# Kernel optimization log

Hardware: AMD Instinct MI355X
Metric: run time of the kernel (lower is better)

The kernel has to match this reference:

```python
import jax, jax.numpy as jnp
import numpy as np
from jax import lax

EPS = 1e-5  # BatchNorm1d default eps

def setup_inputs() -> dict:
    key = jax.random.key(0)
    ks = jax.random.split(key, 8)
    B, IN, H, T = 1024, 128, 256, 256
    return {
        "inputs": jax.random.normal(ks[0], (B, IN), jnp.float32),
        "hidden": jnp.zeros((B, H), jnp.float32),
        "W_ih": jax.random.normal(ks[1], (3 * H, IN), jnp.float32) * 0.05,
        "b_ih": jax.random.normal(ks[2], (3 * H,), jnp.float32) * 0.05,
        "W_hh": jax.random.normal(ks[3], (3 * H, H), jnp.float32) * 0.05,
        "b_hh": jax.random.normal(ks[4], (3 * H,), jnp.float32) * 0.05,
        "W_lin": jax.random.normal(ks[5], (IN, H), jnp.float32) * 0.05,
        "b_lin": jax.random.normal(ks[6], (IN,), jnp.float32) * 0.05,
        "n_frames": 256,
    }

def reference(inputs, hidden, W_ih, b_ih, W_hh, b_hh, W_lin, b_lin, n_frames):
    def step(carry, _):
        x, h = carry
        gi = x @ W_ih.T + b_ih          # [B, 3H]
        gh = h @ W_hh.T + b_hh          # [B, 3H]
        i_r, i_z, i_n = jnp.split(gi, 3, axis=-1)
        h_r, h_z, h_n = jnp.split(gh, 3, axis=-1)
        r = jax.nn.sigmoid(i_r + h_r)
        z = jax.nn.sigmoid(i_z + h_z)
        n = jnp.tanh(i_n + r * h_n)
        h_new = (1.0 - z) * n + z * h   # GRUCell update
        y = h_new @ W_lin.T + b_lin     # fed back as next input
        return (y, h_new), y

    _, ys = lax.scan(step, (inputs, hidden), None, length=n_frames)  # [T, B, out]
    # BatchNorm1d(affine=False), training mode: biased batch stats per timestep
    mean = jnp.mean(ys, axis=1, keepdims=True)
    var = jnp.var(ys, axis=1, keepdims=True)
    return (ys - mean) / jnp.sqrt(var + EPS)
```

## Files before the change

kernel.cpp:

```cpp
#include <hip/hip_runtime.h>


typedef _Float16 half8 __attribute__((ext_vector_type(8)));
typedef float floatx4 __attribute__((ext_vector_type(4)));
typedef unsigned uintx4 __attribute__((ext_vector_type(4)));

#define EPS_BN 1e-5f

#define WS_WC 0
#define WS_W0 524288
#define WS_WL 1114112
#define WS_B0 1179648
#define WS_BC 1183744
#define WS_ST 1187840

static __device__ __forceinline__ unsigned short f2h(float f) {
    union { _Float16 h; unsigned short u; } v;
    v.h = (_Float16)f;
    return v.u;
}
static __device__ __forceinline__ half8 as_h8(uint4 v) {
    union { uint4 u; half8 h; } x; x.u = v; return x.h;
}
static __device__ __forceinline__ half8 ld_agpr(const uint4* p) {
    uintx4 v = *(const uintx4*)p;
    asm volatile("; wpin" : "+a"(v));
    union { uintx4 u; half8 h; } x; x.u = v; return x.h;
}
static __device__ __forceinline__ float sigm(float x) {
    return 1.0f / (1.0f + __expf(-x));
}
static __device__ __forceinline__ float tanh_fast(float x) {
    return 1.0f - 2.0f / (__expf(2.0f * x) + 1.0f);
}
#define MFMA16(A, B, C) __builtin_amdgcn_mfma_f32_16x16x32_f16((A), (B), (C), 0, 0, 0)

__global__ void pack_w0_kernel(const float* __restrict__ W_ih, const float* __restrict__ W_hh,
                               const float* __restrict__ W_lin, const float* __restrict__ b_ih,
                               const float* __restrict__ b_hh,
                               uint4* __restrict__ w0, uint4* __restrict__ wl,
                               float4* __restrict__ bias0)
{
    int i = blockIdx.x * 256 + threadIdx.x;
    if (i < 36864) {
        int lane = i & 63, tile = i >> 6;
        int w = tile / 36, rem = tile - w * 36;
        int g = rem / 12, kt = rem - g * 12;
        int n = g * 256 + (w << 4) + (lane & 15);
        int k0 = (kt << 5) + ((lane >> 4) << 3);
        const float* p = (k0 < 128) ? (W_ih + n * 128 + k0)
                                    : (W_hh + n * 256 + (k0 - 128));
        unsigned short h[8];
        #pragma unroll
        for (int j = 0; j < 8; ++j) h[j] = f2h(p[j]);
        uint4 v;
        v.x = (unsigned)h[0] | ((unsigned)h[1] << 16);
        v.y = (unsigned)h[2] | ((unsigned)h[3] << 16);
        v.z = (unsigned)h[4] | ((unsigned)h[5] << 16);
        v.w = (unsigned)h[6] | ((unsigned)h[7] << 16);
        w0[i] = v;
    } else if (i < 40960) {
        int i2 = i - 36864;
        int lane = i2 & 63, tile = i2 >> 6;
        int n = (tile >> 3) * 16 + (lane & 15);
        int k0 = ((tile & 7) << 5) + ((lane >> 4) << 3);
        const float* p = W_lin + n * 256 + k0;
        unsigned short h[8];
        #pragma unroll
        for (int j = 0; j < 8; ++j) h[j] = f2h(p[j]);
        uint4 v;
        v.x = (unsigned)h[0] | ((unsigned)h[1] << 16);
        v.y = (unsigned)h[2] | ((unsigned)h[3] << 16);
        v.z = (unsigned)h[4] | ((unsigned)h[5] << 16);
        v.w = (unsigned)h[6] | ((unsigned)h[7] << 16);
        wl[i2] = v;
    } else if (i < 41216) {
        int cb = i - 40960;
        bias0[cb] = make_float4(b_ih[cb] + b_hh[cb],
                                b_ih[256 + cb] + b_hh[256 + cb],
                                b_ih[512 + cb], b_hh[512 + cb]);
    }
}

__global__ void pack_wc_kernel(const float* __restrict__ W_ih, const float* __restrict__ W_hh,
                               const float* __restrict__ W_lin, const float* __restrict__ b_ih,
                               const float* __restrict__ b_hh, const float* __restrict__ b_lin,
                               uint4* __restrict__ wc, float4* __restrict__ bc)
{
    int i = blockIdx.x * 256 + threadIdx.x;
    if (i < 32768) {
        int lane = i & 63, tile = i >> 6;
        int w = tile >> 5, r = tile & 31;
        int g = r >> 3, kt = r & 7;
        int c = (w << 4) + (lane & 15);
        int k0 = (kt << 5) + ((lane >> 4) << 3);
        float s[8];
        if (g == 3) {
            #pragma unroll
            for (int j = 0; j < 8; ++j) s[j] = W_hh[(512 + c) * 256 + k0 + j];
        } else {
            int row = g * 256 + c;
            const float* wi = W_ih + row * 128;
            #pragma unroll
            for (int j = 0; j < 8; ++j) s[j] = 0.0f;
            for (int ii = 0; ii < 128; ++ii) {
                float wv = wi[ii];
                const float* wrow = W_lin + ii * 256 + k0;
                #pragma unroll
                for (int j = 0; j < 8; ++j) s[j] += wv * wrow[j];
            }
            if (g < 2) {
                #pragma unroll
                for (int j = 0; j < 8; ++j) s[j] += W_hh[row * 256 + k0 + j];
            }
        }
        unsigned short h[8];
        #pragma unroll
        for (int j = 0; j < 8; ++j) h[j] = f2h(s[j]);
        uint4 v;
        v.x = (unsigned)h[0] | ((unsigned)h[1] << 16);
        v.y = (unsigned)h[2] | ((unsigned)h[3] << 16);
        v.z = (unsigned)h[4] | ((unsigned)h[5] << 16);
        v.w = (unsigned)h[6] | ((unsigned)h[7] << 16);
        wc[i] = v;
    } else if (i < 33024) {
        int c = i - 32768;
        float d0 = 0.f, d1 = 0.f, d2 = 0.f;
        for (int ii = 0; ii < 128; ++ii) {
            float bl = b_lin[ii];
            d0 += bl * W_ih[c * 128 + ii];
            d1 += bl * W_ih[(256 + c) * 128 + ii];
            d2 += bl * W_ih[(512 + c) * 128 + ii];
        }
        bc[c] = make_float4(b_ih[c] + b_hh[c] + d0,
                            b_ih[256 + c] + b_hh[256 + c] + d1,
                            b_ih[512 + c] + d2,
                            b_hh[512 + c]);
    }
}

__global__ __launch_bounds__(512, 2) void gru_kernel(
    const float* __restrict__ inputs,
    const float* __restrict__ hidden,
    const uint4* __restrict__ wc,
    const uint4* __restrict__ w0,
    const float4* __restrict__ bias0,
    const float4* __restrict__ bcp,
    float* __restrict__ out)
{
    __shared__ uint4 lds[9472];

    const int tid  = threadIdx.x;
    const int lane = tid & 63;
    const int w    = tid >> 6;
    const int quad = lane >> 4;
    const int nc   = lane & 15;
    const int r0   = blockIdx.x << 4;
    const int c0   = (w << 4) + nc;
    const int c1   = 128 + c0;
    const float4 bc0 = bcp[c0];
    const float4 bc1 = bcp[c1];
    const uint4* wcw0 = wc + (size_t)w * 2048;
    const uint4* wcw1 = wc + (size_t)(w + 8) * 2048;

    half8 wr0[8], wz0[8], wr1[8], wz1[8];
    #pragma unroll
    for (int kt = 0; kt < 8; ++kt) {
        wr0[kt] = ld_agpr(&wcw0[kt * 64 + lane]);
        wz0[kt] = ld_agpr(&wcw0[(8 + kt) * 64 + lane]);
        wr1[kt] = ld_agpr(&wcw1[kt * 64 + lane]);
        wz1[kt] = ld_agpr(&wcw1[(8 + kt) * 64 + lane]);
    }

    const int wbase = 1280 + (w << 10);
    #pragma unroll
    for (int i = 0; i < 8; ++i) {
        lds[wbase + (i << 6) + lane]       = wcw0[(18 + i) * 64 + lane];
        lds[wbase + 512 + (i << 6) + lane] = wcw1[(18 + i) * 64 + lane];
    }

    float hreg[8];
    #pragma unroll
    for (int d = 0; d < 4; ++d) {
        hreg[d]     = hidden[(r0 + (quad << 2) + d) * 256 + c0];
        hreg[4 + d] = hidden[(r0 + (quad << 2) + d) * 256 + c1];
    }

    unsigned short* lds_u16 = (unsigned short*)lds;
    const int kp  = ((w & 1) << 4) + nc;
    const int lf  = ((kp >> 3) << 4) + (quad << 2);
    const int hfb0 = (((w >> 1) * 64 + lf) << 3) + (kp & 7);
    const int hfb1 = (((4 + (w >> 1)) * 64 + lf) << 3) + (kp & 7);

    for (int idx = tid; idx < 2048; idx += 512) {
        int ktl = idx >> 8;
        int rem = idx & 255;
        int lfr = rem >> 2, jg = rem & 3;
        int m = lfr & 15;
        int hc = ktl * 32 + (lfr >> 4) * 8 + jg * 2;
        const float* p = hidden + (r0 + m) * 256 + hc;
        unsigned pk = (unsigned)f2h(p[0]) | ((unsigned)f2h(p[1]) << 16);
        ((unsigned*)lds)[(ktl * 64 + lfr) * 4 + jg] = pk;
    }
    for (int idx = tid; idx < 1024; idx += 512) {
        int kt = idx >> 8, lfr = (idx >> 2) & 63, jg = idx & 3;
        int m = lfr & 15;
        int k0 = (kt << 5) + ((lfr >> 4) << 3) + (jg << 1);
        const float* p = inputs + (r0 + m) * 128 + k0;
        unsigned pk = (unsigned)f2h(p[0]) | ((unsigned)f2h(p[1]) << 16);
        ((unsigned*)lds)[(1024 + (kt << 6) + lfr) * 4 + jg] = pk;
    }
    __syncthreads();

    unsigned short* Hout = (unsigned short*)out;

    {
        #pragma unroll
        for (int g2 = 0; g2 < 2; ++g2) {
            const uint4* ww = w0 + (size_t)(g2 ? (w + 8) : w) * 2304;
            floatx4 ar = {0.f,0.f,0.f,0.f}, az = {0.f,0.f,0.f,0.f};
            floatx4 ain = {0.f,0.f,0.f,0.f}, ahn = {0.f,0.f,0.f,0.f};
            #pragma unroll
            for (int kt = 0; kt < 12; ++kt) {
                half8 A = as_h8(kt < 4 ? lds[1024 + (kt << 6) + lane]
                                       : lds[((kt - 4) << 6) + lane]);
                ar = MFMA16(A, as_h8(ww[kt * 64 + lane]), ar);
                az = MFMA16(A, as_h8(ww[(12 + kt) * 64 + lane]), az);
                if (kt < 4)
                    ain = MFMA16(A, as_h8(ww[(24 + kt) * 64 + lane]), ain);
                else
                    ahn = MFMA16(A, as_h8(ww[(24 + kt) * 64 + lane]), ahn);
            }
            const int cc = g2 ? c1 : c0;
            const int hfb = g2 ? hfb1 : hfb0;
            float4 b0 = bias0[cc];
            #pragma unroll
            for (int d = 0; d < 4; ++d) {
                float rr = sigm(ar[d] + b0.x);
                float zz = sigm(az[d] + b0.y);
                float nn = tanh_fast(ain[d] + b0.z + rr * (ahn[d] + b0.w));
                float hnew = (1.0f - zz) * nn + zz * hreg[(g2 << 2) + d];
                hreg[(g2 << 2) + d] = hnew;
                unsigned short hu = f2h(hnew);
                lds_u16[4096 + hfb + (d << 3)] = hu;
                Hout[((size_t)(r0 + (quad << 2) + d) << 8) + cc] = hu;
            }
        }
        __syncthreads();
    }

    for (int t = 1; t < 256; ++t) {
        const int rb   = (t & 1) << 9;
        const int wb16 = (((t + 1) & 1) << 9) << 3;

        const uint4* s0p = wcw0 + lane;
        const uint4* s1p = wcw1 + lane;
        asm("" : "+v"(s0p), "+v"(s1p));

        uint4 a_i0 = s0p[16 * 64], a_i1 = s0p[17 * 64];
        uint4 a_h2 = s0p[26 * 64], a_h3 = s0p[27 * 64];
        uint4 b_i0 = s1p[16 * 64], b_i1 = s1p[17 * 64];
        uint4 b_h2 = s1p[26 * 64], b_h3 = s1p[27 * 64];

        floatx4 ar0 = {0.f,0.f,0.f,0.f}, az0 = {0.f,0.f,0.f,0.f};
        floatx4 ai0 = {0.f,0.f,0.f,0.f}, ah0 = {0.f,0.f,0.f,0.f};
        floatx4 ar1 = {0.f,0.f,0.f,0.f}, az1 = {0.f,0.f,0.f,0.f};
        floatx4 ai1 = {0.f,0.f,0.f,0.f}, ah1 = {0.f,0.f,0.f,0.f};

        uint4 a_h4, a_h5, a_h6, a_h7, b_h4, b_h5, b_h6, b_h7;

        #pragma unroll
        for (int kt = 0; kt < 8; ++kt) {
            half8 A = as_h8(lds[rb + (kt << 6) + lane]);
            if (kt == 1) {
                a_h4 = s0p[28 * 64]; b_h4 = s1p[28 * 64];
                a_h5 = s0p[29 * 64]; b_h5 = s1p[29 * 64];
            }
            if (kt == 3) {
                a_h6 = s0p[30 * 64]; b_h6 = s1p[30 * 64];
                a_h7 = s0p[31 * 64]; b_h7 = s1p[31 * 64];
            }
            ar0 = MFMA16(A, wr0[kt], ar0);
            ar1 = MFMA16(A, wr1[kt], ar1);
            az0 = MFMA16(A, wz0[kt], az0);
            az1 = MFMA16(A, wz1[kt], az1);
            half8 Bi0 = (kt == 0) ? as_h8(a_i0) : (kt == 1) ? as_h8(a_i1)
                       : as_h8(lds[wbase + ((kt - 2) << 6) + lane]);
            half8 Bi1 = (kt == 0) ? as_h8(b_i0) : (kt == 1) ? as_h8(b_i1)
                       : as_h8(lds[wbase + 512 + ((kt - 2) << 6) + lane]);
            ai0 = MFMA16(A, Bi0, ai0);
            ai1 = MFMA16(A, Bi1, ai1);
            half8 Bh0 = (kt < 2)  ? as_h8(lds[wbase + ((6 + kt) << 6) + lane])
                       : (kt == 2) ? as_h8(a_h2) : (kt == 3) ? as_h8(a_h3)
                       : (kt == 4) ? as_h8(a_h4) : (kt == 5) ? as_h8(a_h5)
                       : (kt == 6) ? as_h8(a_h6) : as_h8(a_h7);
            half8 Bh1 = (kt < 2)  ? as_h8(lds[wbase + 512 + ((6 + kt) << 6) + lane])
                       : (kt == 2) ? as_h8(b_h2) : (kt == 3) ? as_h8(b_h3)
                       : (kt == 4) ? as_h8(b_h4) : (kt == 5) ? as_h8(b_h5)
                       : (kt == 6) ? as_h8(b_h6) : as_h8(b_h7);
            ah0 = MFMA16(A, Bh0, ah0);
            ah1 = MFMA16(A, Bh1, ah1);
        }

        const size_t obase = (size_t)t * 1024 + r0 + (quad << 2);
        #pragma unroll
        for (int d = 0; d < 4; ++d) {
            float rr = sigm(ar0[d] + bc0.x);
            float zz = sigm(az0[d] + bc0.y);
            float nn = tanh_fast(ai0[d] + bc0.z + rr * (ah0[d] + bc0.w));
            float hnew = (1.0f - zz) * nn + zz * hreg[d];
            hreg[d] = hnew;
            unsigned short hu = f2h(hnew);
            lds_u16[wb16 + hfb0 + (d << 3)] = hu;
            Hout[((obase + d) << 8) + c0] = hu;
        }
        #pragma unroll
        for (int d = 0; d < 4; ++d) {
            float rr = sigm(ar1[d] + bc1.x);
            float zz = sigm(az1[d] + bc1.y);
            float nn = tanh_fast(ai1[d] + bc1.z + rr * (ah1[d] + bc1.w));
            float hnew = (1.0f - zz) * nn + zz * hreg[4 + d];
            hreg[4 + d] = hnew;
            unsigned short hu = f2h(hnew);
            lds_u16[wb16 + hfb1 + (d << 3)] = hu;
            Hout[((obase + d) << 8) + c1] = hu;
        }
        __syncthreads();
    }
}

__global__ __launch_bounds__(256) void ygemm_kernel(
    const uint4* __restrict__ wl, const float* __restrict__ b_lin,
    float* __restrict__ out, float* __restrict__ stats)
{
    __shared__ unsigned short sh[16 * 264];
    const int tid = threadIdx.x;
    const int t = blockIdx.x >> 6;
    const int r0 = (blockIdx.x & 63) << 4;

    {
        int row = tid >> 4, seg = tid & 15;
        const uint4* src = (const uint4*)((const unsigned short*)out
                         + (((size_t)t << 10) + r0 + row) * 256) + (seg << 1);
        uint4 a = src[0], b = src[1];
        uint4* dst = (uint4*)(sh + row * 264 + (seg << 4));
        dst[0] = a; dst[1] = b;
    }
    __syncthreads();

    const int lane = tid & 63, w = tid >> 6;
    const int quad = lane >> 4, nc = lane & 15;
    const int m = lane & 15, khi = lane >> 4;

    half8 B0[8], B1[8];
    #pragma unroll
    for (int kt = 0; kt < 8; ++kt) {
        B0[kt] = as_h8(wl[(((w << 1) + 0) * 8 + kt) * 64 + lane]);
        B1[kt] = as_h8(wl[(((w << 1) + 1) * 8 + kt) * 64 + lane]);
    }
    floatx4 a0 = {0.f,0.f,0.f,0.f}, a1 = {0.f,0.f,0.f,0.f};
    #pragma unroll
    for (int kt = 0; kt < 8; ++kt) {
        half8 A = *(const half8*)(sh + m * 264 + (kt << 5) + (khi << 3));
        a0 = MFMA16(A, B0[kt], a0);
        a1 = MFMA16(A, B1[kt], a1);
    }
    #pragma unroll
    for (int g = 0; g < 2; ++g) {
        floatx4 acc = g ? a1 : a0;
        int i = (((w << 1) + g) << 4) + nc;
        float bl = b_lin[i];
        float s1 = 0.f, s2 = 0.f;
        float* orow = out + (((size_t)t << 10) + r0 + (quad << 2)) * 128 + i;
        #pragma unroll
        for (int d = 0; d < 4; ++d) {
            float y = acc[d] + bl;
            orow[(size_t)d << 7] = y;
            s1 += y; s2 += y * y;
        }
        s1 += __shfl_xor(s1, 16); s1 += __shfl_xor(s1, 32);
        s2 += __shfl_xor(s2, 16); s2 += __shfl_xor(s2, 32);
        if (lane < 16) {
            int si = ((t << 7) + (((w << 1) + g) << 4) + lane) << 1;
            atomicAdd(&stats[si], s1);
            atomicAdd(&stats[si + 1], s2);
        }
    }
}

__global__ void norm_kernel(float* __restrict__ out, const float* __restrict__ stats)
{
    __shared__ float smean[128], sscale[128];
    int t = blockIdx.x >> 2, q = blockIdx.x & 3;
    int tid = threadIdx.x;
    if (tid < 128) {
        int si = ((t << 7) + tid) << 1;
        float mean = stats[si] * (1.0f / 1024.0f);
        float var = stats[si + 1] * (1.0f / 1024.0f) - mean * mean;
        smean[tid] = mean;
        sscale[tid] = rsqrtf(var + EPS_BN);
    }
    __syncthreads();
    float4* p = (float4*)(out + ((size_t)t << 17) + ((size_t)q << 15));
    for (int i = tid; i < 8192; i += 256) {
        int cc = (i & 31) << 2;
        float4 v = p[i];
        v.x = (v.x - smean[cc])     * sscale[cc];
        v.y = (v.y - smean[cc + 1]) * sscale[cc + 1];
        v.z = (v.z - smean[cc + 2]) * sscale[cc + 2];
        v.w = (v.w - smean[cc + 3]) * sscale[cc + 3];
        p[i] = v;
    }
}

extern "C" void kernel_launch(void* const* d_in, const int* in_sizes, int n_in,
                              void* d_out, int out_size, void* d_ws, size_t ws_size,
                              hipStream_t stream) {
    (void)in_sizes; (void)n_in; (void)out_size; (void)ws_size;
    const float* inputs = (const float*)d_in[0];
    const float* hidden = (const float*)d_in[1];
    const float* W_ih   = (const float*)d_in[2];
    const float* b_ih   = (const float*)d_in[3];
    const float* W_hh   = (const float*)d_in[4];
    const float* b_hh   = (const float*)d_in[5];
    const float* W_lin  = (const float*)d_in[6];
    const float* b_lin  = (const float*)d_in[7];

    char* ws = (char*)d_ws;
    uint4*  wcp   = (uint4*)(ws + WS_WC);
    uint4*  w0p   = (uint4*)(ws + WS_W0);
    uint4*  wlp   = (uint4*)(ws + WS_WL);
    float4* bias0 = (float4*)(ws + WS_B0);
    float4* bcp   = (float4*)(ws + WS_BC);
    float*  stats = (float*)(ws + WS_ST);

    hipMemsetAsync(stats, 0, 262144, stream);
    pack_w0_kernel<<<161, 256, 0, stream>>>(W_ih, W_hh, W_lin, b_ih, b_hh, w0p, wlp, bias0);
    pack_wc_kernel<<<129, 256, 0, stream>>>(W_ih, W_hh, W_lin, b_ih, b_hh, b_lin, wcp, bcp);
    gru_kernel<<<64, 512, 0, stream>>>(inputs, hidden, wcp, w0p, bias0, bcp, (float*)d_out);
    ygemm_kernel<<<16384, 256, 0, stream>>>(wlp, b_lin, (float*)d_out, stats);
    norm_kernel<<<1024, 256, 0, stream>>>((float*)d_out, stats);
}
```

Before: 1.064 ms.

## Fuse output linear projection and batch stats into recurrent GRU kernel

Removes the separate ygemm kernel and the fp16 hidden-state round trip through global memory. Each timestep now also computes y = h·W_linᵀ + b_lin from the LDS-resident h and atomically accumulates the BatchNorm statistics inside the persistent GRU loop. To make room, the register/LDS split of the weights is reorganised: half of every gate's K-tiles sit in AGPRs, and the rest are split between LDS and per-step global loads. It also uses raw exp2/rcp intrinsics for sigmoid/tanh and a barrier that waits only on lgkmcnt. The cost is extra serial MFMA work and global stores on the latency-bound recurrent critical path, in exchange for dropping a 16384-block kernel launch and its memory traffic.

```diff
diff --git a/kernel.cpp b/kernel.cpp
--- a/kernel.cpp
+++ b/kernel.cpp
@@ -28,10 +28,13 @@
     union { uintx4 u; half8 h; } x; x.u = v; return x.h;
 }
 static __device__ __forceinline__ float sigm(float x) {
-    return 1.0f / (1.0f + __expf(-x));
+    return __builtin_amdgcn_rcpf(1.0f + __builtin_amdgcn_exp2f(-1.442695041f * x));
 }
 static __device__ __forceinline__ float tanh_fast(float x) {
-    return 1.0f - 2.0f / (__expf(2.0f * x) + 1.0f);
+    return 1.0f - 2.0f * __builtin_amdgcn_rcpf(1.0f + __builtin_amdgcn_exp2f(2.885390082f * x));
+}
+static __device__ __forceinline__ void bar_lgkm() {
+    asm volatile("s_waitcnt lgkmcnt(0)\n\ts_barrier" ::: "memory");
 }
 #define MFMA16(A, B, C) __builtin_amdgcn_mfma_f32_16x16x32_f16((A), (B), (C), 0, 0, 0)
 
@@ -144,9 +147,12 @@
     const float* __restrict__ hidden,
     const uint4* __restrict__ wc,
     const uint4* __restrict__ w0,
+    const uint4* __restrict__ wl,
     const float4* __restrict__ bias0,
     const float4* __restrict__ bcp,
-    float* __restrict__ out)
+    const float* __restrict__ b_lin,
+    float* __restrict__ out,
+    float* __restrict__ stats)
 {
     __shared__ uint4 lds[9472];
 
@@ -160,24 +166,32 @@
     const int c1   = 128 + c0;
     const float4 bc0 = bcp[c0];
     const float4 bc1 = bcp[c1];
+    const float  bl  = b_lin[c0];
     const uint4* wcw0 = wc + (size_t)w * 2048;
     const uint4* wcw1 = wc + (size_t)(w + 8) * 2048;
 
-    half8 wr0[8], wz0[8], wr1[8], wz1[8];
+    half8 pr0[4], pz0[4], pi0[4], ph0[4], pr1[4], pz1[4], pi1[4], ph1[4];
     #pragma unroll
-    for (int kt = 0; kt < 8; ++kt) {
-        wr0[kt] = ld_agpr(&wcw0[kt * 64 + lane]);
-        wz0[kt] = ld_agpr(&wcw0[(8 + kt) * 64 + lane]);
-        wr1[kt] = ld_agpr(&wcw1[kt * 64 + lane]);
-        wz1[kt] = ld_agpr(&wcw1[(8 + kt) * 64 + lane]);
+    for (int kt = 0; kt < 4; ++kt) {
+        pr0[kt] = ld_agpr(&wcw0[kt * 64 + lane]);
+        pz0[kt] = ld_agpr(&wcw0[(8 + kt) * 64 + lane]);
+        pi0[kt] = ld_agpr(&wcw0[(16 + kt) * 64 + lane]);
+        ph0[kt] = ld_agpr(&wcw0[(24 + kt) * 64 + lane]);
+        pr1[kt] = ld_agpr(&wcw1[kt * 64 + lane]);
+        pz1[kt] = ld_agpr(&wcw1[(8 + kt) * 64 + lane]);
+        pi1[kt] = ld_agpr(&wcw1[(16 + kt) * 64 + lane]);
+        ph1[kt] = ld_agpr(&wcw1[(24 + kt) * 64 + lane]);
     }
 
     const int wbase = 1280 + (w << 10);
     #pragma unroll
-    for (int i = 0; i < 8; ++i) {
-        lds[wbase + (i << 6) + lane]       = wcw0[(18 + i) * 64 + lane];
-        lds[wbase + 512 + (i << 6) + lane] = wcw1[(18 + i) * 64 + lane];
-    }
+    for (int i = 0; i < 4; ++i) {
+        lds[wbase + (i << 6) + lane]       = wcw0[(4 + i) * 64 + lane];
+        lds[wbase + ((4 + i) << 6) + lane] = wcw1[(4 + i) * 64 + lane];
+    }
+    #pragma unroll
+    for (int i = 0; i < 8; ++i)
+        lds[wbase + ((8 + i) << 6) + lane] = wl[(size_t)(w * 8 + i) * 64 + lane];
 
     float hreg[8];
     #pragma unroll
@@ -212,8 +226,6 @@
     }
     __syncthreads();
 
-    unsigned short* Hout = (unsigned short*)out;
-
     {
         #pragma unroll
         for (int g2 = 0; g2 < 2; ++g2) {
@@ -241,12 +253,10 @@
                 float nn = tanh_fast(ain[d] + b0.z + rr * (ahn[d] + b0.w));
                 float hnew = (1.0f - zz) * nn + zz * hreg[(g2 << 2) + d];
                 hreg[(g2 << 2) + d] = hnew;
-                unsigned short hu = f2h(hnew);
-                lds_u16[4096 + hfb + (d << 3)] = hu;
-                Hout[((size_t)(r0 + (quad << 2) + d) << 8) + cc] = hu;
-            }
-        }
-        __syncthreads();
+                lds_u16[4096 + hfb + (d << 3)] = f2h(hnew);
+            }
+        }
+        bar_lgkm();
     }
 
     for (int t = 1; t < 256; ++t) {
@@ -257,131 +267,116 @@
         const uint4* s1p = wcw1 + lane;
         asm("" : "+v"(s0p), "+v"(s1p));
 
-        uint4 a_i0 = s0p[16 * 64], a_i1 = s0p[17 * 64];
-        uint4 a_h2 = s0p[26 * 64], a_h3 = s0p[27 * 64];
-        uint4 b_i0 = s1p[16 * 64], b_i1 = s1p[17 * 64];
-        uint4 b_h2 = s1p[26 * 64], b_h3 = s1p[27 * 64];
-
-        floatx4 ar0 = {0.f,0.f,0.f,0.f}, az0 = {0.f,0.f,0.f,0.f};
-        floatx4 ai0 = {0.f,0.f,0.f,0.f}, ah0 = {0.f,0.f,0.f,0.f};
-        floatx4 ar1 = {0.f,0.f,0.f,0.f}, az1 = {0.f,0.f,0.f,0.f};
-        floatx4 ai1 = {0.f,0.f,0.f,0.f}, ah1 = {0.f,0.f,0.f,0.f};
-
-        uint4 a_h4, a_h5, a_h6, a_h7, b_h4, b_h5, b_h6, b_h7;
-
-        #pragma unroll
-        for (int kt = 0; kt < 8; ++kt) {
+        uint4 sz0[4], si0[4], sh0[4], sz1[4], si1[4], sh1[4];
+        sz0[0] = s0p[12 * 64]; si0[0] = s0p[20 * 64]; sh0[0] = s0p[28 * 64];
+        sz1[0] = s1p[12 * 64]; si1[0] = s1p[20 * 64]; sh1[0] = s1p[28 * 64];
+
+        floatx4 acr0 = {0.f,0.f,0.f,0.f}, acz0 = {0.f,0.f,0.f,0.f};
+        floatx4 aci0 = {0.f,0.f,0.f,0.f}, ach0 = {0.f,0.f,0.f,0.f};
+        floatx4 acr1 = {0.f,0.f,0.f,0.f}, acz1 = {0.f,0.f,0.f,0.f};
+        floatx4 aci1 = {0.f,0.f,0.f,0.f}, ach1 = {0.f,0.f,0.f,0.f};
+
+        #pragma unroll
+        for (int kt = 0; kt < 4; ++kt) {
             half8 A = as_h8(lds[rb + (kt << 6) + lane]);
             if (kt == 1) {
-                a_h4 = s0p[28 * 64]; b_h4 = s1p[28 * 64];
-                a_h5 = s0p[29 * 64]; b_h5 = s1p[29 * 64];
+                sz0[1] = s0p[13 * 64]; si0[1] = s0p[21 * 64]; sh0[1] = s0p[29 * 64];
+                sz1[1] = s1p[13 * 64]; si1[1] = s1p[21 * 64]; sh1[1] = s1p[29 * 64];
+            }
+            if (kt == 2) {
+                sz0[2] = s0p[14 * 64]; si0[2] = s0p[22 * 64]; sh0[2] = s0p[30 * 64];
+                sz1[2] = s1p[14 * 64]; si1[2] = s1p[22 * 64]; sh1[2] = s1p[30 * 64];
             }
             if (kt == 3) {
-                a_h6 = s0p[30 * 64]; b_h6 = s1p[30 * 64];
-                a_h7 = s0p[31 * 64]; b_h7 = s1p[31 * 64];
-            }
-            ar0 = MFMA16(A, wr0[kt], ar0);
-            ar1 = MFMA16(A, wr1[kt], ar1);
-            az0 = MFMA16(A, wz0[kt], az0);
-            az1 = MFMA16(A, wz1[kt], az1);
-            half8 Bi0 = (kt == 0) ? as_h8(a_i0) : (kt == 1) ? as_h8(a_i1)
-                       : as_h8(lds[wbase + ((kt - 2) << 6) + lane]);
-            half8 Bi1 = (kt == 0) ? as_h8(b_i0) : (kt == 1) ? as_h8(b_i1)
-                       : as_h8(lds[wbase + 512 + ((kt - 2) << 6) + lane]);
-            ai0 = MFMA16(A, Bi0, ai0);
-            ai1 = MFMA16(A, Bi1, ai1);
-            half8 Bh0 = (kt < 2)  ? as_h8(lds[wbase + ((6 + kt) << 6) + lane])
-                       : (kt == 2) ? as_h8(a_h2) : (kt == 3) ? as_h8(a_h3)
-                       : (kt == 4) ? as_h8(a_h4) : (kt == 5) ? as_h8(a_h5)
-                       : (kt == 6) ? as_h8(a_h6) : as_h8(a_h7);
-            half8 Bh1 = (kt < 2)  ? as_h8(lds[wbase + 512 + ((6 + kt) << 6) + lane])
-                       : (kt == 2) ? as_h8(b_h2) : (kt == 3) ? as_h8(b_h3)
-                       : (kt == 4) ? as_h8(b_h4) : (kt == 5) ? as_h8(b_h5)
-                       : (kt == 6) ? as_h8(b_h6) : as_h8(b_h7);
-            ah0 = MFMA16(A, Bh0, ah0);
-            ah1 = MFMA16(A, Bh1, ah1);
-        }
-
-        const size_t obase = (size_t)t * 1024 + r0 + (quad << 2);
+                sz0[3] = s0p[15 * 64]; si0[3] = s0p[23 * 64]; sh0[3] = s0p[31 * 64];
+                sz1[3] = s1p[15 * 64]; si1[3] = s1p[23 * 64]; sh1[3] = s1p[31 * 64];
+            }
+            acr0 = MFMA16(A, pr0[kt], acr0);
+            acr1 = MFMA16(A, pr1[kt], acr1);
+            acz0 = MFMA16(A, pz0[kt], acz0);
+            acz1 = MFMA16(A, pz1[kt], acz1);
+            aci0 = MFMA16(A, pi0[kt], aci0);
+            aci1 = MFMA16(A, pi1[kt], aci1);
+            ach0 = MFMA16(A, ph0[kt], ach0);
+            ach1 = MFMA16(A, ph1[kt], ach1);
+        }
+        #pragma unroll
+        for (int kt = 0; kt < 4; ++kt) {
+            half8 A = as_h8(lds[rb + ((4 + kt) << 6) + lane]);
+            acr0 = MFMA16(A, as_h8(lds[wbase + (kt << 6) + lane]), acr0);
+            acr1 = MFMA16(A, as_h8(lds[wbase + ((4 + kt) << 6) + lane]), acr1);
+            acz0 = MFMA16(A, as_h8(sz0[kt]), acz0);
+            acz1 = MFMA16(A, as_h8(sz1[kt]), acz1);
+            aci0 = MFMA16(A, as_h8(si0[kt]), aci0);
+            aci1 = MFMA16(A, as_h8(si1[kt]), aci1);
+            ach0 = MFMA16(A, as_h8(sh0[kt]), ach0);
+            ach1 = MFMA16(A, as_h8(sh1[kt]), ach1);
+        }
+
         #pragma unroll
         for (int d = 0; d < 4; ++d) {
-            float rr = sigm(ar0[d] + bc0.x);
-            float zz = sigm(az0[d] + bc0.y);
-            float nn = tanh_fast(ai0[d] + bc0.z + rr * (ah0[d] + bc0.w));
+            float rr = sigm(acr0[d] + bc0.x);
+            float zz = sigm(acz0[d] + bc0.y);
+            float nn = tanh_fast(aci0[d] + bc0.z + rr * (ach0[d] + bc0.w));
             float hnew = (1.0f - zz) * nn + zz * hreg[d];
             hreg[d] = hnew;
-            unsigned short hu = f2h(hnew);
-            lds_u16[wb16 + hfb0 + (d << 3)] = hu;
-            Hout[((obase + d) << 8) + c0] = hu;
+            lds_u16[wb16 + hfb0 + (d << 3)] = f2h(hnew);
         }
         #pragma unroll
         for (int d = 0; d < 4; ++d) {
-            float rr = sigm(ar1[d] + bc1.x);
-            float zz = sigm(az1[d] + bc1.y);
-            float nn = tanh_fast(ai1[d] + bc1.z + rr * (ah1[d] + bc1.w));
+            float rr = sigm(acr1[d] + bc1.x);
+            float zz = sigm(acz1[d] + bc1.y);
+            float nn = tanh_fast(aci1[d] + bc1.z + rr * (ach1[d] + bc1.w));
             float hnew = (1.0f - zz) * nn + zz * hreg[4 + d];
             hreg[4 + d] = hnew;
-            unsigned short hu = f2h(hnew);
-            lds_u16[wb16 + hfb1 + (d << 3)] = hu;
-            Hout[((obase + d) << 8) + c1] = hu;
-        }
-        __syncthreads();
-    }
-}
-
-__global__ __launch_bounds__(256) void ygemm_kernel(
-    const uint4* __restrict__ wl, const float* __restrict__ b_lin,
-    float* __restrict__ out, float* __restrict__ stats)
-{
-    __shared__ unsigned short sh[16 * 264];
-    const int tid = threadIdx.x;
-    const int t = blockIdx.x >> 6;
-    const int r0 = (blockIdx.x & 63) << 4;
+            lds_u16[wb16 + hfb1 + (d << 3)] = f2h(hnew);
+        }
+
+        {
+            floatx4 acy = {0.f,0.f,0.f,0.f};
+            #pragma unroll
+            for (int kt = 0; kt < 8; ++kt) {
+                half8 A = as_h8(lds[rb + (kt << 6) + lane]);
+                acy = MFMA16(A, as_h8(lds[wbase + ((8 + kt) << 6) + lane]), acy);
+            }
+            float s1 = 0.f, s2 = 0.f;
+            float* orow = out + ((size_t)(t - 1) * 1024 + r0 + (quad << 2)) * 128 + c0;
+            #pragma unroll
+            for (int d = 0; d < 4; ++d) {
+                float y = acy[d] + bl;
+                orow[(size_t)d << 7] = y;
+                s1 += y; s2 += y * y;
+            }
+            s1 += __shfl_xor(s1, 16); s1 += __shfl_xor(s1, 32);
+            s2 += __shfl_xor(s2, 16); s2 += __shfl_xor(s2, 32);
+            if (lane < 16) {
+                int si = (((t - 1) << 7) + (w << 4) + lane) << 1;
+                atomicAdd(&stats[si], s1);
+                atomicAdd(&stats[si + 1], s2);
+            }
+        }
+        bar_lgkm();
+    }
 
     {
-        int row = tid >> 4, seg = tid & 15;
-        const uint4* src = (const uint4*)((const unsigned short*)out
-                         + (((size_t)t << 10) + r0 + row) * 256) + (seg << 1);
-        uint4 a = src[0], b = src[1];
-        uint4* dst = (uint4*)(sh + row * 264 + (seg << 4));
-        dst[0] = a; dst[1] = b;
-    }
-    __syncthreads();
-
-    const int lane = tid & 63, w = tid >> 6;
-    const int quad = lane >> 4, nc = lane & 15;
-    const int m = lane & 15, khi = lane >> 4;
-
-    half8 B0[8], B1[8];
-    #pragma unroll
-    for (int kt = 0; kt < 8; ++kt) {
-        B0[kt] = as_h8(wl[(((w << 1) + 0) * 8 + kt) * 64 + lane]);
-        B1[kt] = as_h8(wl[(((w << 1) + 1) * 8 + kt) * 64 + lane]);
-    }
-    floatx4 a0 = {0.f,0.f,0.f,0.f}, a1 = {0.f,0.f,0.f,0.f};
-    #pragma unroll
-    for (int kt = 0; kt < 8; ++kt) {
-        half8 A = *(const half8*)(sh + m * 264 + (kt << 5) + (khi << 3));
-        a0 = MFMA16(A, B0[kt], a0);
-        a1 = MFMA16(A, B1[kt], a1);
-    }
-    #pragma unroll
-    for (int g = 0; g < 2; ++g) {
-        floatx4 acc = g ? a1 : a0;
-        int i = (((w << 1) + g) << 4) + nc;
-        float bl = b_lin[i];
+        floatx4 acy = {0.f,0.f,0.f,0.f};
+        #pragma unroll
+        for (int kt = 0; kt < 8; ++kt) {
+            half8 A = as_h8(lds[(kt << 6) + lane]);
+            acy = MFMA16(A, as_h8(lds[wbase + ((8 + kt) << 6) + lane]), acy);
+        }
         float s1 = 0.f, s2 = 0.f;
-        float* orow = out + (((size_t)t << 10) + r0 + (quad << 2)) * 128 + i;
+        float* orow = out + ((size_t)255 * 1024 + r0 + (quad << 2)) * 128 + c0;
         #pragma unroll
         for (int d = 0; d < 4; ++d) {
-            float y = acc[d] + bl;
+            float y = acy[d] + bl;
             orow[(size_t)d << 7] = y;
             s1 += y; s2 += y * y;
         }
         s1 += __shfl_xor(s1, 16); s1 += __shfl_xor(s1, 32);
         s2 += __shfl_xor(s2, 16); s2 += __shfl_xor(s2, 32);
         if (lane < 16) {
-            int si = ((t << 7) + (((w << 1) + g) << 4) + lane) << 1;
+            int si = ((255 << 7) + (w << 4) + lane) << 1;
             atomicAdd(&stats[si], s1);
             atomicAdd(&stats[si + 1], s2);
         }
@@ -437,7 +432,7 @@
     hipMemsetAsync(stats, 0, 262144, stream);
     pack_w0_kernel<<<161, 256, 0, stream>>>(W_ih, W_hh, W_lin, b_ih, b_hh, w0p, wlp, bias0);
     pack_wc_kernel<<<129, 256, 0, stream>>>(W_ih, W_hh, W_lin, b_ih, b_hh, b_lin, wcp, bcp);
-    gru_kernel<<<64, 512, 0, stream>>>(inputs, hidden, wcp, w0p, bias0, bcp, (float*)d_out);
-    ygemm_kernel<<<16384, 256, 0, stream>>>(wlp, b_lin, (float*)d_out, stats);
+    gru_kernel<<<64, 512, 0, stream>>>(inputs, hidden, wcp, w0p, wlp, bias0, bcp, b_lin,
+                                       (float*)d_out, stats);
     norm_kernel<<<1024, 256, 0, stream>>>((float*)d_out, stats);
 }
```

Measured after the change: 1.508 ms. 41.8% more time.

## Restage weight split between LDS and L2, use raw exp2/rcp, lighter barrier

Applied to the files above, without the earlier changes.

Changes which weight tiles for the input-n and hidden-n gates are kept in LDS (first four k-tiles) versus streamed from global each step (last four), so the global loads issue earlier and have more MFMA work to hide behind. Replaces the sigmoid and tanh with exp2 and hardware reciprocal intrinsics, and swaps __syncthreads for a barrier that waits only on LDS counters, so outstanding global stores no longer stall each recurrent step. The exchange is slightly lower activation precision and a dependence on inline asm for memory ordering.

```diff
diff --git a/kernel.cpp b/kernel.cpp
--- a/kernel.cpp
+++ b/kernel.cpp
@@ -28,10 +28,13 @@
     union { uintx4 u; half8 h; } x; x.u = v; return x.h;
 }
 static __device__ __forceinline__ float sigm(float x) {
-    return 1.0f / (1.0f + __expf(-x));
+    return __builtin_amdgcn_rcpf(1.0f + __builtin_amdgcn_exp2f(-1.442695041f * x));
 }
 static __device__ __forceinline__ float tanh_fast(float x) {
-    return 1.0f - 2.0f / (__expf(2.0f * x) + 1.0f);
+    return 1.0f - 2.0f * __builtin_amdgcn_rcpf(1.0f + __builtin_amdgcn_exp2f(2.885390082f * x));
+}
+static __device__ __forceinline__ void bar_lgkm() {
+    asm volatile("s_waitcnt lgkmcnt(0)\n\ts_barrier" ::: "memory");
 }
 #define MFMA16(A, B, C) __builtin_amdgcn_mfma_f32_16x16x32_f16((A), (B), (C), 0, 0, 0)
 
@@ -174,9 +177,11 @@
 
     const int wbase = 1280 + (w << 10);
     #pragma unroll
-    for (int i = 0; i < 8; ++i) {
-        lds[wbase + (i << 6) + lane]       = wcw0[(18 + i) * 64 + lane];
-        lds[wbase + 512 + (i << 6) + lane] = wcw1[(18 + i) * 64 + lane];
+    for (int i = 0; i < 4; ++i) {
+        lds[wbase + (i << 6) + lane]             = wcw0[(16 + i) * 64 + lane];
+        lds[wbase + ((4 + i) << 6) + lane]       = wcw0[(24 + i) * 64 + lane];
+        lds[wbase + 512 + (i << 6) + lane]       = wcw1[(16 + i) * 64 + lane];
+        lds[wbase + 512 + ((4 + i) << 6) + lane] = wcw1[(24 + i) * 64 + lane];
     }
 
     float hreg[8];
@@ -246,7 +251,7 @@
                 Hout[((size_t)(r0 + (quad << 2) + d) << 8) + cc] = hu;
             }
         }
-        __syncthreads();
+        bar_lgkm();
     }
 
     for (int t = 1; t < 256; ++t) {
@@ -257,47 +262,44 @@
         const uint4* s1p = wcw1 + lane;
         asm("" : "+v"(s0p), "+v"(s1p));
 
-        uint4 a_i0 = s0p[16 * 64], a_i1 = s0p[17 * 64];
-        uint4 a_h2 = s0p[26 * 64], a_h3 = s0p[27 * 64];
-        uint4 b_i0 = s1p[16 * 64], b_i1 = s1p[17 * 64];
-        uint4 b_h2 = s1p[26 * 64], b_h3 = s1p[27 * 64];
+        uint4 si0[4], sh0[4], si1[4], sh1[4];
+        si0[0] = s0p[20 * 64]; sh0[0] = s0p[28 * 64];
+        si1[0] = s1p[20 * 64]; sh1[0] = s1p[28 * 64];
 
         floatx4 ar0 = {0.f,0.f,0.f,0.f}, az0 = {0.f,0.f,0.f,0.f};
         floatx4 ai0 = {0.f,0.f,0.f,0.f}, ah0 = {0.f,0.f,0.f,0.f};
         floatx4 ar1 = {0.f,0.f,0.f,0.f}, az1 = {0.f,0.f,0.f,0.f};
         floatx4 ai1 = {0.f,0.f,0.f,0.f}, ah1 = {0.f,0.f,0.f,0.f};
 
-        uint4 a_h4, a_h5, a_h6, a_h7, b_h4, b_h5, b_h6, b_h7;
-
         #pragma unroll
         for (int kt = 0; kt < 8; ++kt) {
             half8 A = as_h8(lds[rb + (kt << 6) + lane]);
             if (kt == 1) {
-                a_h4 = s0p[28 * 64]; b_h4 = s1p[28 * 64];
-                a_h5 = s0p[29 * 64]; b_h5 = s1p[29 * 64];
+                si0[1] = s0p[21 * 64]; sh0[1] = s0p[29 * 64];
+                si1[1] = s1p[21 * 64]; sh1[1] = s1p[29 * 64];
+            }
+            if (kt == 2) {
+                si0[2] = s0p[22 * 64]; sh0[2] = s0p[30 * 64];
+                si1[2] = s1p[22 * 64]; sh1[2] = s1p[30 * 64];
             }
             if (kt == 3) {
-                a_h6 = s0p[30 * 64]; b_h6 = s1p[30 * 64];
-                a_h7 = s0p[31 * 64]; b_h7 = s1p[31 * 64];
+                si0[3] = s0p[23 * 64]; sh0[3] = s0p[31 * 64];
+                si1[3] = s1p[23 * 64]; sh1[3] = s1p[31 * 64];
             }
             ar0 = MFMA16(A, wr0[kt], ar0);
             ar1 = MFMA16(A, wr1[kt], ar1);
             az0 = MFMA16(A, wz0[kt], az0);
             az1 = MFMA16(A, wz1[kt], az1);
-            half8 Bi0 = (kt == 0) ? as_h8(a_i0) : (kt == 1) ? as_h8(a_i1)
-                       : as_h8(lds[wbase + ((kt - 2) << 6) + lane]);
-            half8 Bi1 = (kt == 0) ? as_h8(b_i0) : (kt == 1) ? as_h8(b_i1)
-                       : as_h8(lds[wbase + 512 + ((kt - 2) << 6) + lane]);
+            half8 Bi0 = (kt < 4) ? as_h8(lds[wbase + (kt << 6) + lane])
+                                 : as_h8(si0[kt - 4]);
+            half8 Bi1 = (kt < 4) ? as_h8(lds[wbase + 512 + (kt << 6) + lane])
+                                 : as_h8(si1[kt - 4]);
             ai0 = MFMA16(A, Bi0, ai0);
             ai1 = MFMA16(A, Bi1, ai1);
-            half8 Bh0 = (kt < 2)  ? as_h8(lds[wbase + ((6 + kt) << 6) + lane])
-                       : (kt == 2) ? as_h8(a_h2) : (kt == 3) ? as_h8(a_h3)
-                       : (kt == 4) ? as_h8(a_h4) : (kt == 5) ? as_h8(a_h5)
-                       : (kt == 6) ? as_h8(a_h6) : as_h8(a_h7);
-            half8 Bh1 = (kt < 2)  ? as_h8(lds[wbase + 512 + ((6 + kt) << 6) + lane])
-                       : (kt == 2) ? as_h8(b_h2) : (kt == 3) ? as_h8(b_h3)
-                       : (kt == 4) ? as_h8(b_h4) : (kt == 5) ? as_h8(b_h5)
-                       : (kt == 6) ? as_h8(b_h6) : as_h8(b_h7);
+            half8 Bh0 = (kt < 4) ? as_h8(lds[wbase + ((4 + kt) << 6) + lane])
+                                 : as_h8(sh0[kt - 4]);
+            half8 Bh1 = (kt < 4) ? as_h8(lds[wbase + 512 + ((4 + kt) << 6) + lane])
+                                 : as_h8(sh1[kt - 4]);
             ah0 = MFMA16(A, Bh0, ah0);
             ah1 = MFMA16(A, Bh1, ah1);
         }
@@ -325,7 +327,7 @@
             lds_u16[wb16 + hfb1 + (d << 3)] = hu;
             Hout[((obase + d) << 8) + c1] = hu;
         }
-        __syncthreads();
+        bar_lgkm();
     }
 }
 
```

Result: no change. 1.047 ms (-1.5%).
